# Kernel optimization log

Hardware: AMD Instinct MI355X
Metric: run time of the kernel (lower is better)

The kernel has to match this reference:

```python
import jax, jax.numpy as jnp
import numpy as np

N_NODES = 100000
N_EDGES = 600000
IN_DIM = 128
HID = 128
N_GRAPHS = 512
N_CLASSES = 10


def setup_inputs() -> dict:
    key = jax.random.key(0)
    ks = jax.random.split(key, 8)
    feats = jax.random.normal(ks[0], (N_NODES, IN_DIM), dtype=jnp.float32)
    W = jax.random.normal(ks[1], (IN_DIM, HID), dtype=jnp.float32) * 0.05
    b = jnp.zeros((HID,), dtype=jnp.float32)
    W1 = jax.random.normal(ks[2], (HID, 12), dtype=jnp.float32) * 0.05
    b1 = jnp.zeros((12,), dtype=jnp.float32)
    W2 = jax.random.normal(ks[3], (12, N_CLASSES), dtype=jnp.float32) * 0.05
    b2 = jnp.zeros((N_CLASSES,), dtype=jnp.float32)
    src = jax.random.randint(ks[4], (N_EDGES,), 0, N_NODES, dtype=jnp.int32)
    dst = jax.random.randint(ks[5], (N_EDGES,), 0, N_NODES, dtype=jnp.int32)
    graph_ids = jnp.sort(jax.random.randint(ks[6], (N_NODES,), 0, N_GRAPHS, dtype=jnp.int32))
    return {"feats": feats, "W": W, "b": b, "W1": W1, "b1": b1, "W2": W2,
            "b2": b2, "src": src, "dst": dst, "graph_ids": graph_ids}


def reference(feats, W, b, W1, b1, W2, b2, src, dst, graph_ids):
    ones_e = jnp.ones((src.shape[0],), dtype=feats.dtype)
    # DGL GraphConv norm='both': clamp degrees to >= 1
    out_deg = jnp.maximum(jax.ops.segment_sum(ones_e, src, num_segments=N_NODES), 1.0)
    in_deg = jnp.maximum(jax.ops.segment_sum(ones_e, dst, num_segments=N_NODES), 1.0)
    norm_src = out_deg ** -0.5  # [N]
    norm_dst = in_deg ** -0.5
    x = feats * norm_src[:, None]               # scale source features
    agg = jax.ops.segment_sum(x[src], dst, num_segments=N_NODES)  # gather-scatter SpMM
    h = agg * norm_dst[:, None]
    h = jnp.maximum(h @ W + b, 0.0)             # GraphConv linear + ReLU  [N, HID]
    # mean_nodes: per-graph segment mean (empty graphs -> 0, matching DGL)
    gsum = jax.ops.segment_sum(h, graph_ids, num_segments=N_GRAPHS)
    cnt = jax.ops.segment_sum(jnp.ones((N_NODES,), h.dtype), graph_ids, num_segments=N_GRAPHS)
    hg = jnp.where(cnt[:, None] > 0, gsum / jnp.maximum(cnt, 1.0)[:, None], 0.0)
    # tiny 2-layer MLP classifier
    return (hg @ W1 + b1) @ W2 + b2             # [N_GRAPHS, N_CLASSES]
```

## Files before the change

kernel.cpp:

```cpp
#include <hip/hip_runtime.h>
#include <hip/hip_fp16.h>

#define N_NODES 100000
#define N_EDGES 600000
#define DIM 128
#define N_GRAPHS 512
#define MLP_HID 12
#define N_CLASSES 10
#define NPB 16
#define SLOT_CAP 32
#define TPAD 136

#define WFRAG_BLOCKS 8
#define EDGE1_BLOCKS ((N_EDGES + 255) / 256)
#define CONV_BLOCKS 6250

typedef _Float16 half8 __attribute__((ext_vector_type(8)));
typedef float float4v __attribute__((ext_vector_type(4)));
typedef float floatx2 __attribute__((ext_vector_type(2)));

__global__ void prep1_kernel(const int* __restrict__ src, const int* __restrict__ dst,
                             int* __restrict__ out_hist, int* __restrict__ in_hist,
                             int* __restrict__ slots,
                             const float* __restrict__ W, __half* __restrict__ wfrag) {
    int bx = blockIdx.x;
    if (bx < WFRAG_BLOCKS) {
        int item = bx * 256 + threadIdx.x;
        if (item < 2048) {
            int lane = item & 63;
            int kt = (item >> 6) & 3;
            int nt = item >> 8;
            int n = nt * 16 + (lane & 15);
            int k0 = kt * 32 + (lane >> 4) * 8;
            union { int4 i4; __half h[8]; } u;
            #pragma unroll
            for (int j = 0; j < 8; ++j) u.h[j] = __float2half(W[(k0 + j) * DIM + n]);
            ((int4*)wfrag)[item] = u.i4;
        }
        return;
    }
    int i = (bx - WFRAG_BLOCKS) * 256 + threadIdx.x;
    if (i < N_EDGES) {
        int s = src[i];
        int d = dst[i];
        atomicAdd(&out_hist[s], 1);
        int tk = atomicAdd(&in_hist[d], 1);
        if (tk < SLOT_CAP) slots[d * SLOT_CAP + tk] = s;
    }
}

__global__ void prep2_kernel(const float4* __restrict__ feats4, int2* __restrict__ feats_q,
                             const int* __restrict__ out_hist) {
    int i = blockIdx.x * 256 + threadIdx.x;
    int n = i >> 4;
    float ns = rsqrtf((float)max(out_hist[n], 1));
    float4 a = feats4[2 * i];
    float4 c = feats4[2 * i + 1];
    int lo = __builtin_amdgcn_cvt_pk_fp8_f32(a.x * ns, a.y * ns, 0, false);
    lo     = __builtin_amdgcn_cvt_pk_fp8_f32(a.z * ns, a.w * ns, lo, true);
    int hi = __builtin_amdgcn_cvt_pk_fp8_f32(c.x * ns, c.y * ns, 0, false);
    hi     = __builtin_amdgcn_cvt_pk_fp8_f32(c.z * ns, c.w * ns, hi, true);
    feats_q[i] = make_int2(lo, hi);
}

__global__ __launch_bounds__(128) void fused_gemm(
        const int* __restrict__ feats_q,
        const int* __restrict__ in_hist, const int* __restrict__ slots,
        const __half* __restrict__ wfrag,
        const float* __restrict__ bvec, const int* __restrict__ gid,
        float* __restrict__ gsum, float* __restrict__ cnt) {
    __shared__ __half tile_h[NPB][TPAD];
    int t = threadIdx.x;
    int group = t >> 5;
    int lane = t & 31;
    int node0 = blockIdx.x * NPB;

    int dv = 0;
    if (lane < 16) dv = in_hist[node0 + lane];
    int deg[4]; int es[4];
    #pragma unroll
    for (int r = 0; r < 4; ++r) {
        int j = r * 4 + group;
        deg[r] = __shfl(dv, j, 32);
        es[r] = 0;
        if (lane < min(deg[r], SLOT_CAP)) es[r] = slots[(node0 + j) * SLOT_CAP + lane];
    }

    #pragma unroll
    for (int r = 0; r < 4; ++r) {
        int j = r * 4 + group;
        int m = min(deg[r], SLOT_CAP);
        float4 a4 = make_float4(0.f, 0.f, 0.f, 0.f);
        int i = 0;
        for (; i + 4 <= m; i += 4) {
            int sn0 = __shfl(es[r], i + 0, 32), sn1 = __shfl(es[r], i + 1, 32);
            int sn2 = __shfl(es[r], i + 2, 32), sn3 = __shfl(es[r], i + 3, 32);
            int q0 = feats_q[sn0 * 32 + lane];
            int q1 = feats_q[sn1 * 32 + lane];
            int q2 = feats_q[sn2 * 32 + lane];
            int q3 = feats_q[sn3 * 32 + lane];
            floatx2 p0 = __builtin_amdgcn_cvt_pk_f32_fp8(q0, false);
            floatx2 r0 = __builtin_amdgcn_cvt_pk_f32_fp8(q0, true);
            floatx2 p1 = __builtin_amdgcn_cvt_pk_f32_fp8(q1, false);
            floatx2 r1 = __builtin_amdgcn_cvt_pk_f32_fp8(q1, true);
            floatx2 p2 = __builtin_amdgcn_cvt_pk_f32_fp8(q2, false);
            floatx2 r2 = __builtin_amdgcn_cvt_pk_f32_fp8(q2, true);
            floatx2 p3 = __builtin_amdgcn_cvt_pk_f32_fp8(q3, false);
            floatx2 r3 = __builtin_amdgcn_cvt_pk_f32_fp8(q3, true);
            a4.x += p0[0] + p1[0] + p2[0] + p3[0];
            a4.y += p0[1] + p1[1] + p2[1] + p3[1];
            a4.z += r0[0] + r1[0] + r2[0] + r3[0];
            a4.w += r0[1] + r1[1] + r2[1] + r3[1];
        }
        for (; i < m; ++i) {
            int sn = __shfl(es[r], i, 32);
            int q = feats_q[sn * 32 + lane];
            floatx2 p = __builtin_amdgcn_cvt_pk_f32_fp8(q, false);
            floatx2 rr = __builtin_amdgcn_cvt_pk_f32_fp8(q, true);
            a4.x += p[0]; a4.y += p[1]; a4.z += rr[0]; a4.w += rr[1];
        }
        float nd = rsqrtf((float)max(deg[r], 1));
        union { int2 v; __half2 h2[2]; } st;
        st.h2[0] = __floats2half2_rn(a4.x * nd, a4.y * nd);
        st.h2[1] = __floats2half2_rn(a4.z * nd, a4.w * nd);
        *(int2*)&tile_h[j][lane * 4] = st.v;
    }
    __syncthreads();

    int wave = t >> 6;
    int wl = t & 63;
    int quad = wl >> 4;
    int col = wl & 15;

    half8 afrag[4];
    #pragma unroll
    for (int kt = 0; kt < 4; ++kt)
        afrag[kt] = *reinterpret_cast<const half8*>(&tile_h[col][kt * 32 + quad * 8]);

    float4v c[4];
    #pragma unroll
    for (int nt = 0; nt < 4; ++nt) { c[nt][0] = 0.f; c[nt][1] = 0.f; c[nt][2] = 0.f; c[nt][3] = 0.f; }

    #pragma unroll
    for (int nt = 0; nt < 4; ++nt) {
        int ntile = wave * 4 + nt;
        #pragma unroll
        for (int kt = 0; kt < 4; ++kt) {
            half8 bfrag = *reinterpret_cast<const half8*>(wfrag + ((size_t)(ntile * 4 + kt) * 64 + wl) * 8);
            c[nt] = __builtin_amdgcn_mfma_f32_16x16x32_f16(afrag[kt], bfrag, c[nt], 0, 0, 0);
        }
    }

    int g0 = gid[node0];
    if (gid[node0 + NPB - 1] == g0) {
        #pragma unroll
        for (int nt = 0; nt < 4; ++nt) {
            float bb = bvec[(wave * 4 + nt) * 16 + col];
            float v = 0.f;
            #pragma unroll
            for (int i2 = 0; i2 < 4; ++i2) v += fmaxf(c[nt][i2] + bb, 0.f);
            v += __shfl_xor(v, 16, 64);
            v += __shfl_xor(v, 32, 64);
            if (wl < 16) atomicAdd(&gsum[g0 * DIM + (wave * 4 + nt) * 16 + col], v);
        }
        if (t == 0) atomicAdd(&cnt[g0], (float)NPB);
    } else {
        #pragma unroll
        for (int nt = 0; nt < 4; ++nt) {
            float bb = bvec[(wave * 4 + nt) * 16 + col];
            #pragma unroll
            for (int i2 = 0; i2 < 4; ++i2) {
                int g = gid[node0 + quad * 4 + i2];
                atomicAdd(&gsum[g * DIM + (wave * 4 + nt) * 16 + col],
                          fmaxf(c[nt][i2] + bb, 0.f));
            }
        }
        if (wave == 0 && col == 0) {
            #pragma unroll
            for (int i2 = 0; i2 < 4; ++i2)
                atomicAdd(&cnt[gid[node0 + quad * 4 + i2]], 1.0f);
        }
    }
}

__global__ __launch_bounds__(128) void mlp_kernel(
        const float* __restrict__ gsum, const float* __restrict__ cnt,
        const float* __restrict__ W1, const float* __restrict__ b1,
        const float* __restrict__ W2, const float* __restrict__ b2,
        float* __restrict__ out) {
    __shared__ float s[DIM];
    __shared__ float t1[MLP_HID];
    int g = blockIdx.x;
    int t = threadIdx.x;
    float c = cnt[g];
    s[t] = (c > 0.0f) ? (gsum[g * DIM + t] / c) : 0.0f;
    __syncthreads();
    if (t < MLP_HID) {
        float a = b1[t];
        for (int k = 0; k < DIM; ++k) a = fmaf(s[k], W1[k * MLP_HID + t], a);
        t1[t] = a;
    }
    __syncthreads();
    if (t < N_CLASSES) {
        float o = b2[t];
        #pragma unroll
        for (int j = 0; j < MLP_HID; ++j) o = fmaf(t1[j], W2[j * N_CLASSES + t], o);
        out[g * N_CLASSES + t] = o;
    }
}

extern "C" void kernel_launch(void* const* d_in, const int* in_sizes, int n_in,
                              void* d_out, int out_size, void* d_ws, size_t ws_size,
                              hipStream_t stream) {
    const float* feats = (const float*)d_in[0];
    const float* W     = (const float*)d_in[1];
    const float* b     = (const float*)d_in[2];
    const float* W1    = (const float*)d_in[3];
    const float* b1    = (const float*)d_in[4];
    const float* W2    = (const float*)d_in[5];
    const float* b2    = (const float*)d_in[6];
    const int*   src   = (const int*)d_in[7];
    const int*   dst   = (const int*)d_in[8];
    const int*   gid   = (const int*)d_in[9];
    float* out = (float*)d_out;

    char* ws = (char*)d_ws;
    int*   out_hist = (int*)ws;   ws += (size_t)N_NODES * 4;
    int*   in_hist  = (int*)ws;   ws += (size_t)N_NODES * 4;
    float* gsum     = (float*)ws; ws += (size_t)N_GRAPHS * DIM * 4;
    float* cnt      = (float*)ws; ws += (size_t)N_GRAPHS * 4;
    size_t zero_bytes = (size_t)(ws - (char*)d_ws);
    ws = (char*)(((uintptr_t)ws + 255) & ~(uintptr_t)255);
    int*    slots   = (int*)ws;    ws += (size_t)N_NODES * SLOT_CAP * 4;
    int*    feats_q = (int*)ws;    ws += (size_t)N_NODES * DIM;
    __half* wfrag   = (__half*)ws; ws += (size_t)2048 * 8 * 2;

    hipMemsetAsync(d_ws, 0, zero_bytes, stream);

    prep1_kernel<<<WFRAG_BLOCKS + EDGE1_BLOCKS, 256, 0, stream>>>(
        src, dst, out_hist, in_hist, slots, W, wfrag);

    prep2_kernel<<<CONV_BLOCKS, 256, 0, stream>>>(
        (const float4*)feats, (int2*)feats_q, out_hist);

    fused_gemm<<<N_NODES / NPB, 128, 0, stream>>>(
        feats_q, in_hist, slots, wfrag, b, gid, gsum, cnt);

    mlp_kernel<<<N_GRAPHS, 128, 0, stream>>>(gsum, cnt, W1, b1, W2, b2, out);
}
```

Before: 214.6 us.

## Merge prep kernels by moving source-degree scaling into the gather

FP8 quantization of features no longer depends on out-degree, so it is merged with the edge histogram and W-fragment kernel into one launch, removing a kernel boundary and serialization. The per-source normalization is now applied in the gather loop by loading out_hist per neighbor and using FMAs. Edge processing handles two edges per thread with nontemporal slot stores. The trade-offs are an extra scattered load per edge in the hot kernel and quantizing unscaled features, which slightly changes FP8 precision.

```diff
diff --git a/kernel.cpp b/kernel.cpp
--- a/kernel.cpp
+++ b/kernel.cpp
@@ -12,17 +12,19 @@
 #define TPAD 136
 
 #define WFRAG_BLOCKS 8
-#define EDGE1_BLOCKS ((N_EDGES + 255) / 256)
 #define CONV_BLOCKS 6250
+#define EDGE2_ITEMS (N_EDGES / 2)
+#define EDGE2_BLOCKS ((EDGE2_ITEMS + 255) / 256)
 
 typedef _Float16 half8 __attribute__((ext_vector_type(8)));
 typedef float float4v __attribute__((ext_vector_type(4)));
 typedef float floatx2 __attribute__((ext_vector_type(2)));
 
-__global__ void prep1_kernel(const int* __restrict__ src, const int* __restrict__ dst,
-                             int* __restrict__ out_hist, int* __restrict__ in_hist,
-                             int* __restrict__ slots,
-                             const float* __restrict__ W, __half* __restrict__ wfrag) {
+__global__ void prep_kernel(const float* __restrict__ W, __half* __restrict__ wfrag,
+                            const float4* __restrict__ feats4, int2* __restrict__ feats_q,
+                            const int* __restrict__ src, const int* __restrict__ dst,
+                            int* __restrict__ out_hist, int* __restrict__ in_hist,
+                            int* __restrict__ slots) {
     int bx = blockIdx.x;
     if (bx < WFRAG_BLOCKS) {
         int item = bx * 256 + threadIdx.x;
@@ -39,34 +41,36 @@
         }
         return;
     }
-    int i = (bx - WFRAG_BLOCKS) * 256 + threadIdx.x;
-    if (i < N_EDGES) {
-        int s = src[i];
-        int d = dst[i];
-        atomicAdd(&out_hist[s], 1);
-        int tk = atomicAdd(&in_hist[d], 1);
-        if (tk < SLOT_CAP) slots[d * SLOT_CAP + tk] = s;
-    }
-}
-
-__global__ void prep2_kernel(const float4* __restrict__ feats4, int2* __restrict__ feats_q,
-                             const int* __restrict__ out_hist) {
-    int i = blockIdx.x * 256 + threadIdx.x;
-    int n = i >> 4;
-    float ns = rsqrtf((float)max(out_hist[n], 1));
-    float4 a = feats4[2 * i];
-    float4 c = feats4[2 * i + 1];
-    int lo = __builtin_amdgcn_cvt_pk_fp8_f32(a.x * ns, a.y * ns, 0, false);
-    lo     = __builtin_amdgcn_cvt_pk_fp8_f32(a.z * ns, a.w * ns, lo, true);
-    int hi = __builtin_amdgcn_cvt_pk_fp8_f32(c.x * ns, c.y * ns, 0, false);
-    hi     = __builtin_amdgcn_cvt_pk_fp8_f32(c.z * ns, c.w * ns, hi, true);
-    feats_q[i] = make_int2(lo, hi);
+    bx -= WFRAG_BLOCKS;
+    if (bx < CONV_BLOCKS) {
+        int i = bx * 256 + threadIdx.x;
+        float4 a = feats4[2 * i];
+        float4 c = feats4[2 * i + 1];
+        int lo = __builtin_amdgcn_cvt_pk_fp8_f32(a.x, a.y, 0, false);
+        lo     = __builtin_amdgcn_cvt_pk_fp8_f32(a.z, a.w, lo, true);
+        int hi = __builtin_amdgcn_cvt_pk_fp8_f32(c.x, c.y, 0, false);
+        hi     = __builtin_amdgcn_cvt_pk_fp8_f32(c.z, c.w, hi, true);
+        feats_q[i] = make_int2(lo, hi);
+        return;
+    }
+    bx -= CONV_BLOCKS;
+    int i = bx * 256 + threadIdx.x;
+    if (i < EDGE2_ITEMS) {
+        int2 s2 = ((const int2*)src)[i];
+        int2 d2 = ((const int2*)dst)[i];
+        atomicAdd(&out_hist[s2.x], 1);
+        atomicAdd(&out_hist[s2.y], 1);
+        int t0 = atomicAdd(&in_hist[d2.x], 1);
+        int t1 = atomicAdd(&in_hist[d2.y], 1);
+        if (t0 < SLOT_CAP) __builtin_nontemporal_store(s2.x, &slots[d2.x * SLOT_CAP + t0]);
+        if (t1 < SLOT_CAP) __builtin_nontemporal_store(s2.y, &slots[d2.y * SLOT_CAP + t1]);
+    }
 }
 
 __global__ __launch_bounds__(128) void fused_gemm(
         const int* __restrict__ feats_q,
-        const int* __restrict__ in_hist, const int* __restrict__ slots,
-        const __half* __restrict__ wfrag,
+        const int* __restrict__ in_hist, const int* __restrict__ out_hist,
+        const int* __restrict__ slots, const __half* __restrict__ wfrag,
         const float* __restrict__ bvec, const int* __restrict__ gid,
         float* __restrict__ gsum, float* __restrict__ cnt) {
     __shared__ __half tile_h[NPB][TPAD];
@@ -84,6 +88,12 @@
         deg[r] = __shfl(dv, j, 32);
         es[r] = 0;
         if (lane < min(deg[r], SLOT_CAP)) es[r] = slots[(node0 + j) * SLOT_CAP + lane];
+    }
+    float ns[4];
+    #pragma unroll
+    for (int r = 0; r < 4; ++r) {
+        ns[r] = 0.0f;
+        if (lane < min(deg[r], SLOT_CAP)) ns[r] = rsqrtf((float)max(out_hist[es[r]], 1));
     }
 
     #pragma unroll
@@ -95,6 +105,8 @@
         for (; i + 4 <= m; i += 4) {
             int sn0 = __shfl(es[r], i + 0, 32), sn1 = __shfl(es[r], i + 1, 32);
             int sn2 = __shfl(es[r], i + 2, 32), sn3 = __shfl(es[r], i + 3, 32);
+            float n0 = __shfl(ns[r], i + 0, 32), n1 = __shfl(ns[r], i + 1, 32);
+            float n2 = __shfl(ns[r], i + 2, 32), n3 = __shfl(ns[r], i + 3, 32);
             int q0 = feats_q[sn0 * 32 + lane];
             int q1 = feats_q[sn1 * 32 + lane];
             int q2 = feats_q[sn2 * 32 + lane];
@@ -107,17 +119,23 @@
             floatx2 r2 = __builtin_amdgcn_cvt_pk_f32_fp8(q2, true);
             floatx2 p3 = __builtin_amdgcn_cvt_pk_f32_fp8(q3, false);
             floatx2 r3 = __builtin_amdgcn_cvt_pk_f32_fp8(q3, true);
-            a4.x += p0[0] + p1[0] + p2[0] + p3[0];
-            a4.y += p0[1] + p1[1] + p2[1] + p3[1];
-            a4.z += r0[0] + r1[0] + r2[0] + r3[0];
-            a4.w += r0[1] + r1[1] + r2[1] + r3[1];
+            a4.x = fmaf(p0[0], n0, a4.x); a4.y = fmaf(p0[1], n0, a4.y);
+            a4.z = fmaf(r0[0], n0, a4.z); a4.w = fmaf(r0[1], n0, a4.w);
+            a4.x = fmaf(p1[0], n1, a4.x); a4.y = fmaf(p1[1], n1, a4.y);
+            a4.z = fmaf(r1[0], n1, a4.z); a4.w = fmaf(r1[1], n1, a4.w);
+            a4.x = fmaf(p2[0], n2, a4.x); a4.y = fmaf(p2[1], n2, a4.y);
+            a4.z = fmaf(r2[0], n2, a4.z); a4.w = fmaf(r2[1], n2, a4.w);
+            a4.x = fmaf(p3[0], n3, a4.x); a4.y = fmaf(p3[1], n3, a4.y);
+            a4.z = fmaf(r3[0], n3, a4.z); a4.w = fmaf(r3[1], n3, a4.w);
         }
         for (; i < m; ++i) {
             int sn = __shfl(es[r], i, 32);
+            float nv = __shfl(ns[r], i, 32);
             int q = feats_q[sn * 32 + lane];
             floatx2 p = __builtin_amdgcn_cvt_pk_f32_fp8(q, false);
             floatx2 rr = __builtin_amdgcn_cvt_pk_f32_fp8(q, true);
-            a4.x += p[0]; a4.y += p[1]; a4.z += rr[0]; a4.w += rr[1];
+            a4.x = fmaf(p[0], nv, a4.x); a4.y = fmaf(p[1], nv, a4.y);
+            a4.z = fmaf(rr[0], nv, a4.z); a4.w = fmaf(rr[1], nv, a4.w);
         }
         float nd = rsqrtf((float)max(deg[r], 1));
         union { int2 v; __half2 h2[2]; } st;
@@ -237,14 +255,12 @@
 
     hipMemsetAsync(d_ws, 0, zero_bytes, stream);
 
-    prep1_kernel<<<WFRAG_BLOCKS + EDGE1_BLOCKS, 256, 0, stream>>>(
-        src, dst, out_hist, in_hist, slots, W, wfrag);
-
-    prep2_kernel<<<CONV_BLOCKS, 256, 0, stream>>>(
-        (const float4*)feats, (int2*)feats_q, out_hist);
+    prep_kernel<<<WFRAG_BLOCKS + CONV_BLOCKS + EDGE2_BLOCKS, 256, 0, stream>>>(
+        W, wfrag, (const float4*)feats, (int2*)feats_q,
+        src, dst, out_hist, in_hist, slots);
 
     fused_gemm<<<N_NODES / NPB, 128, 0, stream>>>(
-        feats_q, in_hist, slots, wfrag, b, gid, gsum, cnt);
+        feats_q, in_hist, out_hist, slots, wfrag, b, gid, gsum, cnt);
 
     mlp_kernel<<<N_GRAPHS, 128, 0, stream>>>(gsum, cnt, W1, b1, W2, b2, out);
 }
```

Measured after the change: 217.5 us. About the same (+1.3%).
